# Performance work log

Hardware: AMD Instinct MI355X
Metric: run time of the kernel (lower is better)

The kernel has to match this reference:

```python
import jax, jax.numpy as jnp
import numpy as np

EMBED_DIM = 768
NUM_HEADS = 12
HEAD_DIM = EMBED_DIM // NUM_HEADS
MLP_HIDDEN = int(EMBED_DIM * 4.0)
LN_EPS = 1e-5


def setup_inputs() -> dict:
    key = jax.random.key(0)
    ks = jax.random.split(key, 8)
    C, H = EMBED_DIM, MLP_HIDDEN
    s = 0.02
    return {
        "x": jax.random.normal(ks[0], (2, 2048, C), dtype=jnp.float32),
        "ln1_g": jnp.ones((C,), jnp.float32),
        "ln1_b": jnp.zeros((C,), jnp.float32),
        "qkv_w": jax.random.normal(ks[1], (3 * C, C), jnp.float32) * s,
        "proj_w": jax.random.normal(ks[2], (C, C), jnp.float32) * s,
        "proj_b": jnp.zeros((C,), jnp.float32),
        "ln2_g": jnp.ones((C,), jnp.float32),
        "ln2_b": jnp.zeros((C,), jnp.float32),
        "fc1_w": jax.random.normal(ks[3], (H, C), jnp.float32) * s,
        "fc1_b": jnp.zeros((H,), jnp.float32),
        "fc2_w": jax.random.normal(ks[4], (C, H), jnp.float32) * s,
        "fc2_b": jnp.zeros((C,), jnp.float32),
    }


def _layernorm(x, g, b):
    mu = jnp.mean(x, axis=-1, keepdims=True)
    var = jnp.mean(jnp.square(x - mu), axis=-1, keepdims=True)
    return (x - mu) * jax.lax.rsqrt(var + LN_EPS) * g + b


def reference(x, ln1_g, ln1_b, qkv_w, proj_w, proj_b, ln2_g, ln2_b,
              fc1_w, fc1_b, fc2_w, fc2_b):
    B, N, C = x.shape
    Hh, Dh = NUM_HEADS, HEAD_DIM
    scale = Dh ** -0.5

    # --- attention branch (pre-norm) ---
    h = _layernorm(x, ln1_g, ln1_b)
    qkv = h @ qkv_w.T                                   # [B,N,3C]
    qkv = qkv.reshape(B, N, 3, Hh, Dh)
    q = qkv[:, :, 0].transpose(0, 2, 1, 3)              # [B,H,N,D]
    k = qkv[:, :, 1].transpose(0, 2, 1, 3)
    v = qkv[:, :, 2].transpose(0, 2, 1, 3)
    attn = jnp.einsum('bhnd,bhmd->bhnm', q, k) * scale  # [B,H,N,N]
    attn = jax.nn.softmax(attn, axis=-1)
    o = jnp.einsum('bhnm,bhmd->bhnd', attn, v)          # [B,H,N,D]
    o = o.transpose(0, 2, 1, 3).reshape(B, N, C)
    x = x + o @ proj_w.T + proj_b

    # --- MLP branch (pre-norm), exact GELU like nn.GELU ---
    h = _layernorm(x, ln2_g, ln2_b)
    h = jax.nn.gelu(h @ fc1_w.T + fc1_b, approximate=False)
    x = x + h @ fc2_w.T + fc2_b
    return x
```

## Files before the change

### kernel.cpp

```cpp
#include <hip/hip_runtime.h>
#include <hip/hip_bf16.h>
#include <cstdint>
#include <math.h>


typedef __bf16 bf16_t;
typedef bf16_t bf16x4 __attribute__((ext_vector_type(4)));
typedef bf16_t bf16x8 __attribute__((ext_vector_type(8)));
typedef float floatx4 __attribute__((ext_vector_type(4)));

#define AS1 __attribute__((address_space(1)))
#define AS3 __attribute__((address_space(3)))

__device__ __forceinline__ void async_load16(const void* g, void* l) {
  const AS1 unsigned int* gp =
      reinterpret_cast<const AS1 unsigned int*>(reinterpret_cast<uintptr_t>(g));
  AS3 unsigned int* lp = reinterpret_cast<AS3 unsigned int*>(
      static_cast<unsigned int>(reinterpret_cast<uintptr_t>(l)));
  __builtin_amdgcn_global_load_lds(gp, lp, 16, 0, 0);
}

__device__ __forceinline__ bf16x8 lds_read8(const bf16_t* p) {
  return *reinterpret_cast<const bf16x8*>(p);
}

__global__ __launch_bounds__(256) void cvt_k(const float* __restrict__ in,
                                             bf16_t* __restrict__ out, int n4) {
  const int i = blockIdx.x * 256 + threadIdx.x;
  if (i < n4) {
    const float4 v = reinterpret_cast<const float4*>(in)[i];
    bf16x4 o;
    o[0] = (bf16_t)v.x; o[1] = (bf16_t)v.y; o[2] = (bf16_t)v.z; o[3] = (bf16_t)v.w;
    reinterpret_cast<bf16x4*>(out)[i] = o;
  }
}

__global__ __launch_bounds__(256) void cvt_all_k(
    const float* __restrict__ s0, const float* __restrict__ s1,
    const float* __restrict__ s2, const float* __restrict__ s3,
    bf16_t* __restrict__ d0, bf16_t* __restrict__ d1, bf16_t* __restrict__ d2,
    bf16_t* __restrict__ d3) {
  int i = blockIdx.x * 256 + threadIdx.x;
  const float* src;
  bf16_t* dst;
  if (i < 442368) { src = s0; dst = d0; }
  else if (i < 589824) { src = s1; dst = d1; i -= 442368; }
  else if (i < 1179648) { src = s2; dst = d2; i -= 589824; }
  else if (i < 1769472) { src = s3; dst = d3; i -= 1179648; }
  else return;
  const float4 v = reinterpret_cast<const float4*>(src)[i];
  bf16x4 o;
  o[0] = (bf16_t)v.x; o[1] = (bf16_t)v.y; o[2] = (bf16_t)v.z; o[3] = (bf16_t)v.w;
  reinterpret_cast<bf16x4*>(dst)[i] = o;
}

__global__ __launch_bounds__(256) void ln_k(const float* __restrict__ x,
                                            const float* __restrict__ g,
                                            const float* __restrict__ b,
                                            bf16_t* __restrict__ out) {
  const int row = blockIdx.x;
  const int tid = threadIdx.x;
  const float* xr = x + (long)row * 768;
  float v[3];
#pragma unroll
  for (int e = 0; e < 3; e++) v[e] = xr[tid + e * 256];
  float s = v[0] + v[1] + v[2];
  float ss = v[0] * v[0] + v[1] * v[1] + v[2] * v[2];
#pragma unroll
  for (int off = 32; off >= 1; off >>= 1) {
    s += __shfl_down(s, off, 64);
    ss += __shfl_down(ss, off, 64);
  }
  __shared__ float red[8];
  __shared__ float stat[2];
  const int wv = tid >> 6;
  if ((tid & 63) == 0) { red[wv] = s; red[4 + wv] = ss; }
  __syncthreads();
  if (tid == 0) {
    float S = red[0] + red[1] + red[2] + red[3];
    float SS = red[4] + red[5] + red[6] + red[7];
    float mu = S * (1.0f / 768.0f);
    float var = SS * (1.0f / 768.0f) - mu * mu;
    stat[0] = mu;
    stat[1] = rsqrtf(var + 1e-5f);
  }
  __syncthreads();
  const float mu = stat[0], rs = stat[1];
#pragma unroll
  for (int e = 0; e < 3; e++) {
    int c = tid + e * 256;
    out[(long)row * 768 + c] = (bf16_t)((v[e] - mu) * rs * g[c] + b[c]);
  }
}

template <int MODE>
__global__ __launch_bounds__(256, 2) void gemm_k(
    const bf16_t* __restrict__ A, const bf16_t* __restrict__ Bt, int lda,
    int ldb, int keff, int Nld, const float* __restrict__ bias,
    bf16_t* __restrict__ out_bf, bf16_t* __restrict__ q_out,
    bf16_t* __restrict__ k_out, bf16_t* __restrict__ vt_out) {
  constexpr int BK = 32;
  __shared__ __align__(16) bf16_t As[2][128 * BK];
  __shared__ __align__(16) bf16_t Bs[2][128 * BK];

  const int tid = threadIdx.x;
  const int w = tid >> 6;
  const int lane = tid & 63;
  const int quad = lane >> 4;
  const int lid = lane & 15;
  const int wr = (w >> 1) * 64;
  const int wc = (w & 1) * 64;
  const int mBase = blockIdx.y * 128;
  const int nBase = blockIdx.x * 128;

  const int ldsRowSub = lane >> 2;
  const int kblk = (lane & 3) ^ (ldsRowSub & 3);
  const int rq0 = (quad ^ (lid & 3)) * 8;
  const int c0 = w * 2, c1 = w * 2 + 1;
  const int rowA0 = c0 * 16 + ldsRowSub, rowA1 = c1 * 16 + ldsRowSub;

  const bf16_t* Ag = A + (long)mBase * lda;
  const bf16_t* Bg = Bt + (long)nBase * ldb;

  floatx4 acc[4][4];
#pragma unroll
  for (int i = 0; i < 4; i++)
#pragma unroll
    for (int j = 0; j < 4; j++) acc[i][j] = (floatx4){0.f, 0.f, 0.f, 0.f};

  async_load16(Ag + (long)rowA0 * lda + kblk * 8, &As[0][c0 * 512]);
  async_load16(Ag + (long)rowA1 * lda + kblk * 8, &As[0][c1 * 512]);
  async_load16(Bg + (long)rowA0 * ldb + kblk * 8, &Bs[0][c0 * 512]);
  async_load16(Bg + (long)rowA1 * ldb + kblk * 8, &Bs[0][c1 * 512]);

  const int iters = keff / BK;
  int cur = 0;
  for (int it = 0; it < iters; it++) {
    __syncthreads();
    if (it + 1 < iters) {
      const int k0 = (it + 1) * BK;
      const int nb = cur ^ 1;
      async_load16(Ag + (long)rowA0 * lda + k0 + kblk * 8, &As[nb][c0 * 512]);
      async_load16(Ag + (long)rowA1 * lda + k0 + kblk * 8, &As[nb][c1 * 512]);
      async_load16(Bg + (long)rowA0 * ldb + k0 + kblk * 8, &Bs[nb][c0 * 512]);
      async_load16(Bg + (long)rowA1 * ldb + k0 + kblk * 8, &Bs[nb][c1 * 512]);
    }

    bf16x8 af[4], bfv[4];
#pragma unroll
    for (int i = 0; i < 4; i++)
      af[i] = lds_read8(&As[cur][(wr + i * 16 + lid) * BK + rq0]);
#pragma unroll
    for (int j = 0; j < 4; j++)
      bfv[j] = lds_read8(&Bs[cur][(wc + j * 16 + lid) * BK + rq0]);
#pragma unroll
    for (int i = 0; i < 4; i++)
#pragma unroll
      for (int j = 0; j < 4; j++)
        acc[i][j] = __builtin_amdgcn_mfma_f32_16x16x32_bf16(af[i], bfv[j],
                                                            acc[i][j], 0, 0, 0);
    cur ^= 1;
  }

#pragma unroll
  for (int i = 0; i < 4; i++) {
    const int mRow = mBase + wr + i * 16 + quad * 4;
#pragma unroll
    for (int j = 0; j < 4; j++) {
      const int n = nBase + wc + j * 16 + lid;
      if constexpr (MODE == 0) {
        const int which = n / 768;
        const int rem = n - which * 768;
        const int head = rem >> 6;
        const int d = rem & 63;
        const int b = mRow >> 11;
        const int t = mRow & 2047;
        const int bh = b * 12 + head;
        if (which == 2) {
          bf16x4 pk;
#pragma unroll
          for (int r = 0; r < 4; r++) pk[r] = (bf16_t)acc[i][j][r];
          const long off = ((long)bh * 64 + d) * 2048 + t;
          *reinterpret_cast<bf16x4*>(&vt_out[off]) = pk;
        } else if (which == 0) {
#pragma unroll
          for (int r = 0; r < 4; r++)
            q_out[((long)bh * 2048 + t + r) * 64 + d] =
                (bf16_t)(acc[i][j][r] * 0.125f);
        } else {
#pragma unroll
          for (int r = 0; r < 4; r++)
            k_out[((long)bh * 2048 + t + r) * 64 + d] = (bf16_t)acc[i][j][r];
        }
      } else {
        const float bv = bias[n];
#pragma unroll
        for (int r = 0; r < 4; r++) {
          float v = acc[i][j][r] + bv;
          float ge = 0.5f * v * (1.0f + erff(v * 0.70710678118654752f));
          out_bf[(long)(mRow + r) * Nld + n] = (bf16_t)ge;
        }
      }
    }
  }
}

template <int MODE>
__global__ __launch_bounds__(256, 2) void gemm64_k(
    const bf16_t* __restrict__ A, const bf16_t* __restrict__ Bt, int lda,
    int ldb, int keff, int Nld, const float* __restrict__ bias,
    const float* __restrict__ resid_f, float* __restrict__ out_f) {
  constexpr int BK = 32;
  __shared__ __align__(16) bf16_t As[2][128 * BK];
  __shared__ __align__(16) bf16_t Bs[2][64 * BK];

  const int tid = threadIdx.x;
  const int w = tid >> 6;
  const int lane = tid & 63;
  const int quad = lane >> 4;
  const int lid = lane & 15;
  const int mBase = blockIdx.y * 128;
  const int nBase = blockIdx.x * 64;

  const int ldsRowSub = lane >> 2;
  const int kblk = (lane & 3) ^ (ldsRowSub & 3);
  const int rq0 = (quad ^ (lid & 3)) * 8;
  const int rowA0 = w * 16 + ldsRowSub;
  const int rowA1 = (w + 4) * 16 + ldsRowSub;

  const bf16_t* Ag = A + (long)mBase * lda;
  const bf16_t* Bg = Bt + (long)nBase * ldb;

  floatx4 acc[2][4];
#pragma unroll
  for (int i = 0; i < 2; i++)
#pragma unroll
    for (int j = 0; j < 4; j++) acc[i][j] = (floatx4){0.f, 0.f, 0.f, 0.f};

  async_load16(Ag + (long)rowA0 * lda + kblk * 8, &As[0][w * 512]);
  async_load16(Ag + (long)rowA1 * lda + kblk * 8, &As[0][(w + 4) * 512]);
  async_load16(Bg + (long)rowA0 * ldb + kblk * 8, &Bs[0][w * 512]);

  const int iters = keff / BK;
  int cur = 0;
  for (int it = 0; it < iters; it++) {
    __syncthreads();
    if (it + 1 < iters) {
      const int k0 = (it + 1) * BK;
      const int nb = cur ^ 1;
      async_load16(Ag + (long)rowA0 * lda + k0 + kblk * 8, &As[nb][w * 512]);
      async_load16(Ag + (long)rowA1 * lda + k0 + kblk * 8, &As[nb][(w + 4) * 512]);
      async_load16(Bg + (long)rowA0 * ldb + k0 + kblk * 8, &Bs[nb][w * 512]);
    }

    bf16x8 af[2], bfv[4];
#pragma unroll
    for (int i = 0; i < 2; i++)
      af[i] = lds_read8(&As[cur][(w * 32 + i * 16 + lid) * BK + rq0]);
#pragma unroll
    for (int j = 0; j < 4; j++)
      bfv[j] = lds_read8(&Bs[cur][(j * 16 + lid) * BK + rq0]);
#pragma unroll
    for (int i = 0; i < 2; i++)
#pragma unroll
      for (int j = 0; j < 4; j++)
        acc[i][j] = __builtin_amdgcn_mfma_f32_16x16x32_bf16(af[i], bfv[j],
                                                            acc[i][j], 0, 0, 0);
    cur ^= 1;
  }

#pragma unroll
  for (int i = 0; i < 2; i++) {
    const int mRow = mBase + w * 32 + i * 16 + quad * 4;
#pragma unroll
    for (int j = 0; j < 4; j++) {
      const int n = nBase + j * 16 + lid;
      if constexpr (MODE == 1) {
        const float bv = bias[n];
#pragma unroll
        for (int r = 0; r < 4; r++) {
          const long off = (long)(mRow + r) * Nld + n;
          out_f[off] = resid_f[off] + acc[i][j][r] + bv;
        }
      } else {
#pragma unroll
        for (int r = 0; r < 4; r++) {
          const long off = (long)(mRow + r) * Nld + n;
          out_f[off] += acc[i][j][r];
        }
      }
    }
  }
}

__global__ __launch_bounds__(512, 1) void flash_k(const bf16_t* __restrict__ q,
                                                  const bf16_t* __restrict__ kk,
                                                  const bf16_t* __restrict__ vt,
                                                  bf16_t* __restrict__ U,
                                                  float* __restrict__ lbuf) {
  constexpr int SK = 64, D = 64, PS = 68;
  __shared__ __align__(16) bf16_t Ks[2][SK * D];
  __shared__ __align__(16) bf16_t Vs[2][D * SK];
  __shared__ __align__(16) bf16_t Ps[8][16 * PS];

  const int tid = threadIdx.x;
  const int w = tid >> 6;
  const int lane = tid & 63;
  const int quad = lane >> 4;
  const int lid = lane & 15;
  const int bh = blockIdx.y;
  const int half = blockIdx.z;
  const int qBase = blockIdx.x * 128;

  const bf16_t* qg = q + ((long)bh * 2048 + qBase) * D;
  const bf16_t* kg = kk + ((long)bh * 2048 + half * 1024) * D;
  const bf16_t* vg = vt + (long)bh * D * 2048 + half * 1024;

  bf16x8 aq[2];
#pragma unroll
  for (int k2 = 0; k2 < 2; k2++)
    aq[k2] = *reinterpret_cast<const bf16x8*>(qg + (w * 16 + lid) * D +
                                              k2 * 32 + quad * 8);

  const int srow = lane >> 3;
  const int sdb = (lane & 7) ^ srow;
  const int rsw = lid & 7;

  async_load16(kg + (long)(w * 8 + srow) * D + sdb * 8, &Ks[0][w * 512]);
  async_load16(vg + (long)(w * 8 + srow) * 2048 + sdb * 8, &Vs[0][w * 512]);

  float lsum = 0.f;
  floatx4 oacc[4];
#pragma unroll
  for (int jo = 0; jo < 4; jo++) oacc[jo] = (floatx4){0.f, 0.f, 0.f, 0.f};

  int cur = 0;
  for (int kci = 0; kci < 16; kci++) {
    __syncthreads();
    if (kci + 1 < 16) {
      const int kc = (kci + 1) * 64;
      const int nb = cur ^ 1;
      async_load16(kg + (long)(kc + w * 8 + srow) * D + sdb * 8, &Ks[nb][w * 512]);
      async_load16(vg + (long)(w * 8 + srow) * 2048 + kc + sdb * 8, &Vs[nb][w * 512]);
    }

    floatx4 sacc[4];
#pragma unroll
    for (int jm = 0; jm < 4; jm++) sacc[jm] = (floatx4){0.f, 0.f, 0.f, 0.f};
#pragma unroll
    for (int k2 = 0; k2 < 2; k2++) {
#pragma unroll
      for (int jm = 0; jm < 4; jm++) {
        const bf16x8 ak = lds_read8(
            &Ks[cur][(jm * 16 + lid) * D + (((k2 * 4 + quad) ^ rsw) * 8)]);
        sacc[jm] =
            __builtin_amdgcn_mfma_f32_16x16x32_bf16(ak, aq[k2], sacc[jm], 0, 0, 0);
      }
    }

#pragma unroll
    for (int jm = 0; jm < 4; jm++) {
      bf16x4 pk;
      float ps = 0.f;
#pragma unroll
      for (int r = 0; r < 4; r++) {
        const float p = exp2f(fmaf(sacc[jm][r], 1.44269504f, -11.5415603f));
        ps += p;
        pk[r] = (bf16_t)p;
      }
      lsum += ps;
      *reinterpret_cast<bf16x4*>(&Ps[w][lid * PS + jm * 16 + quad * 4]) = pk;
    }

#pragma unroll
    for (int k2 = 0; k2 < 2; k2++) {
      const bf16x8 ap = lds_read8(&Ps[w][lid * PS + k2 * 32 + quad * 8]);
#pragma unroll
      for (int jo = 0; jo < 4; jo++) {
        const bf16x8 bv = lds_read8(
            &Vs[cur][(jo * 16 + lid) * SK + (((k2 * 4 + quad) ^ rsw) * 8)]);
        oacc[jo] =
            __builtin_amdgcn_mfma_f32_16x16x32_bf16(ap, bv, oacc[jo], 0, 0, 0);
      }
    }
    cur ^= 1;
  }

  lsum += __shfl_xor(lsum, 16, 64);
  lsum += __shfl_xor(lsum, 32, 64);

  const long lrow = ((long)half * 24 + bh) * 2048 + qBase + w * 16;
  if (quad == 0) lbuf[lrow + lid] = lsum;

  bf16_t* Ub = U + (((long)half * 24 + bh) * 2048 + qBase) * D;
#pragma unroll
  for (int jo = 0; jo < 4; jo++) {
#pragma unroll
    for (int r = 0; r < 4; r++) {
      const int t = w * 16 + quad * 4 + r;
      Ub[(long)t * D + jo * 16 + lid] = (bf16_t)oacc[jo][r];
    }
  }
}

__global__ __launch_bounds__(256) void combine_k(const bf16_t* __restrict__ U,
                                                 const float* __restrict__ lbuf,
                                                 bf16_t* __restrict__ o) {
  const int idx = blockIdx.x * 256 + threadIdx.x;
  const int bh = idx >> 17;
  const int rem = idx & 131071;
  const int t = rem >> 6;
  const int d = rem & 63;
  const float l0 = lbuf[bh * 2048 + t];
  const float l1 = lbuf[(24 + bh) * 2048 + t];
  const float u = (float)U[idx] + (float)U[3145728 + idx];
  const int b = bh / 12;
  const int head = bh - b * 12;
  o[((long)b * 2048 + t) * 768 + head * 64 + d] = (bf16_t)(u / (l0 + l1));
}

extern "C" void kernel_launch(void* const* d_in, const int* in_sizes, int n_in,
                              void* d_out, int out_size, void* d_ws,
                              size_t ws_size, hipStream_t stream) {
  (void)in_sizes; (void)n_in; (void)out_size;
  const float* x = (const float*)d_in[0];
  const float* ln1_g = (const float*)d_in[1];
  const float* ln1_b = (const float*)d_in[2];
  const float* qkv_w = (const float*)d_in[3];
  const float* proj_w = (const float*)d_in[4];
  const float* proj_b = (const float*)d_in[5];
  const float* ln2_g = (const float*)d_in[6];
  const float* ln2_b = (const float*)d_in[7];
  const float* fc1_w = (const float*)d_in[8];
  const float* fc1_b = (const float*)d_in[9];
  const float* fc2_w = (const float*)d_in[10];
  const float* fc2_b = (const float*)d_in[11];
  float* out = (float*)d_out;
  char* ws = (char*)d_ws;

  const bool big = ws_size >= (size_t)64487424;

  if (big) {
    bf16_t* wqkv = (bf16_t*)(ws + 0);
    bf16_t* wproj = (bf16_t*)(ws + 3538944);
    bf16_t* wfc1 = (bf16_t*)(ws + 4718592);
    bf16_t* wfc2 = (bf16_t*)(ws + 9437184);
    bf16_t* h1 = (bf16_t*)(ws + 14155776);
    bf16_t* ob = h1;
    bf16_t* qb = (bf16_t*)(ws + 20447232);
    bf16_t* kb = (bf16_t*)(ws + 26738688);
    bf16_t* vtb = (bf16_t*)(ws + 33030144);
    bf16_t* Ubuf = (bf16_t*)(ws + 39321600);
    float* lbuf = (float*)(ws + 51904512);
    float* x1 = (float*)(ws + 20447232);
    bf16_t* h2 = (bf16_t*)(ws + 33030144);
    bf16_t* hg = (bf16_t*)(ws + 39321600);

    cvt_all_k<<<6912, 256, 0, stream>>>(qkv_w, proj_w, fc1_w, fc2_w, wqkv,
                                        wproj, wfc1, wfc2);
    ln_k<<<4096, 256, 0, stream>>>(x, ln1_g, ln1_b, h1);
    gemm_k<0><<<dim3(18, 32), 256, 0, stream>>>(h1, wqkv, 768, 768, 768, 2304,
                                                nullptr, nullptr, qb, kb, vtb);
    flash_k<<<dim3(16, 24, 2), 512, 0, stream>>>(qb, kb, vtb, Ubuf, lbuf);
    combine_k<<<12288, 256, 0, stream>>>(Ubuf, lbuf, ob);
    gemm64_k<1><<<dim3(12, 32), 256, 0, stream>>>(ob, wproj, 768, 768, 768, 768,
                                                  proj_b, x, x1);
    ln_k<<<4096, 256, 0, stream>>>(x1, ln2_g, ln2_b, h2);
    gemm_k<2><<<dim3(24, 32), 256, 0, stream>>>(h2, wfc1, 768, 768, 768, 3072,
                                                fc1_b, hg, nullptr, nullptr,
                                                nullptr);
    gemm64_k<1><<<dim3(12, 32), 256, 0, stream>>>(hg, wfc2, 3072, 3072, 3072,
                                                  768, fc2_b, x1, out);
  } else {
    bf16_t* wqkv = (bf16_t*)(ws + 0);
    bf16_t* wproj = (bf16_t*)(ws + 3538944);
    bf16_t* h1 = (bf16_t*)(ws + 4718592);
    bf16_t* ob = h1;
    bf16_t* qb = (bf16_t*)(ws + 11010048);
    bf16_t* kb = (bf16_t*)(ws + 17301504);
    bf16_t* vtb = (bf16_t*)(ws + 23592960);
    float* x1 = (float*)(ws + 11010048);
    bf16_t* h2 = (bf16_t*)(ws + 23592960);
    bf16_t* wfc1 = (bf16_t*)(ws + 0);
    bf16_t* wfc2 = (bf16_t*)(ws + 4718592);
    bf16_t* hg = (bf16_t*)(ws + 29884416);
    bf16_t* Ubuf = (bf16_t*)(ws + 29884416);
    float* lbuf = (float*)(ws + 42467328);

    cvt_k<<<1728, 256, 0, stream>>>(qkv_w, wqkv, 442368);
    cvt_k<<<576, 256, 0, stream>>>(proj_w, wproj, 147456);
    ln_k<<<4096, 256, 0, stream>>>(x, ln1_g, ln1_b, h1);
    gemm_k<0><<<dim3(18, 32), 256, 0, stream>>>(h1, wqkv, 768, 768, 768, 2304,
                                                nullptr, nullptr, qb, kb, vtb);
    flash_k<<<dim3(16, 24, 2), 512, 0, stream>>>(qb, kb, vtb, Ubuf, lbuf);
    combine_k<<<12288, 256, 0, stream>>>(Ubuf, lbuf, ob);
    gemm64_k<1><<<dim3(12, 32), 256, 0, stream>>>(ob, wproj, 768, 768, 768, 768,
                                                  proj_b, x, x1);
    cvt_k<<<2304, 256, 0, stream>>>(fc1_w, wfc1, 589824);
    cvt_k<<<2304, 256, 0, stream>>>(fc2_w, wfc2, 589824);
    ln_k<<<4096, 256, 0, stream>>>(x1, ln2_g, ln2_b, h2);
    for (int h = 0; h < 2; h++) {
      gemm_k<2><<<dim3(12, 32), 256, 0, stream>>>(
          h2, wfc1 + (long)h * 1536 * 768, 768, 768, 768, 1536,
          fc1_b + h * 1536, hg, nullptr, nullptr, nullptr);
      if (h == 0)
        gemm64_k<1><<<dim3(12, 32), 256, 0, stream>>>(hg, wfc2 + 0, 1536, 3072,
                                                      1536, 768, fc2_b, x1, out);
      else
        gemm64_k<5><<<dim3(12, 32), 256, 0, stream>>>(hg, wfc2 + 1536, 1536,
                                                      3072, 1536, 768, nullptr,
                                                      nullptr, out);
    }
  }
}
```

Baseline: 293.9 us.

## Keep attention probabilities in registers via permlane swaps instead of LDS

```diff
diff --git a/kernel.cpp b/kernel.cpp
--- a/kernel.cpp
+++ b/kernel.cpp
@@ -94,7 +94,7 @@
 }
 
 template <int MODE>
-__global__ __launch_bounds__(256, 2) void gemm_k(
+__global__ __launch_bounds__(256, 3) void gemm_k(
     const bf16_t* __restrict__ A, const bf16_t* __restrict__ Bt, int lda,
     int ldb, int keff, int Nld, const float* __restrict__ bias,
     bf16_t* __restrict__ out_bf, bf16_t* __restrict__ q_out,
@@ -298,10 +298,9 @@
                                                   const bf16_t* __restrict__ vt,
                                                   bf16_t* __restrict__ U,
                                                   float* __restrict__ lbuf) {
-  constexpr int SK = 64, D = 64, PS = 68;
+  constexpr int SK = 64, D = 64;
   __shared__ __align__(16) bf16_t Ks[2][SK * D];
   __shared__ __align__(16) bf16_t Vs[2][D * SK];
-  __shared__ __align__(16) bf16_t Ps[8][16 * PS];
 
   const int tid = threadIdx.x;
   const int w = tid >> 6;
@@ -358,29 +357,41 @@
       }
     }
 
-#pragma unroll
-    for (int jm = 0; jm < 4; jm++) {
-      bf16x4 pk;
-      float ps = 0.f;
-#pragma unroll
-      for (int r = 0; r < 4; r++) {
-        const float p = exp2f(fmaf(sacc[jm][r], 1.44269504f, -11.5415603f));
-        ps += p;
-        pk[r] = (bf16_t)p;
+    bf16x8 ap[2];
+#pragma unroll
+    for (int k2 = 0; k2 < 2; k2++) {
+      uint32_t pk[2][2];
+#pragma unroll
+      for (int j = 0; j < 2; j++) {
+        const int jm = k2 * 2 + j;
+        const float p0 = exp2f(fmaf(sacc[jm][0], 1.44269504f, -11.5415603f));
+        const float p1 = exp2f(fmaf(sacc[jm][1], 1.44269504f, -11.5415603f));
+        const float p2 = exp2f(fmaf(sacc[jm][2], 1.44269504f, -11.5415603f));
+        const float p3 = exp2f(fmaf(sacc[jm][3], 1.44269504f, -11.5415603f));
+        lsum += ((p0 + p1) + p2) + p3;
+        asm("v_cvt_pk_bf16_f32 %0, %1, %2" : "=v"(pk[j][0]) : "v"(p0), "v"(p1));
+        asm("v_cvt_pk_bf16_f32 %0, %1, %2" : "=v"(pk[j][1]) : "v"(p2), "v"(p3));
       }
-      lsum += ps;
-      *reinterpret_cast<bf16x4*>(&Ps[w][lid * PS + jm * 16 + quad * 4]) = pk;
+      asm("v_permlane32_swap_b32 %0, %1" : "+v"(pk[0][0]), "+v"(pk[1][0]));
+      asm("v_permlane16_swap_b32 %0, %1" : "+v"(pk[0][0]), "+v"(pk[1][0]));
+      asm("v_permlane32_swap_b32 %0, %1" : "+v"(pk[0][1]), "+v"(pk[1][1]));
+      asm("v_permlane16_swap_b32 %0, %1" : "+v"(pk[0][1]), "+v"(pk[1][1]));
+      union { uint32_t u[4]; bf16x8 v; } au;
+      au.u[0] = pk[0][0];
+      au.u[1] = pk[0][1];
+      au.u[2] = pk[1][0];
+      au.u[3] = pk[1][1];
+      ap[k2] = au.v;
     }
 
 #pragma unroll
     for (int k2 = 0; k2 < 2; k2++) {
-      const bf16x8 ap = lds_read8(&Ps[w][lid * PS + k2 * 32 + quad * 8]);
 #pragma unroll
       for (int jo = 0; jo < 4; jo++) {
         const bf16x8 bv = lds_read8(
             &Vs[cur][(jo * 16 + lid) * SK + (((k2 * 4 + quad) ^ rsw) * 8)]);
         oacc[jo] =
-            __builtin_amdgcn_mfma_f32_16x16x32_bf16(ap, bv, oacc[jo], 0, 0, 0);
+            __builtin_amdgcn_mfma_f32_16x16x32_bf16(ap[k2], bv, oacc[jo], 0, 0, 0);
       }
     }
     cur ^= 1;
```

New measurement: 284.6 us. -3.2%, faster.
